# Kernel tuning notes

Hardware: AMD Instinct MI355X
Metric: run time of the kernel (lower is better)

## Reference

```python
import jax, jax.numpy as jnp
import numpy as np

B, T, H, IN, OUT, FUT = 256, 512, 512, 1, 1, 16


def setup_inputs() -> dict:
    key = jax.random.key(0)
    ks = jax.random.split(key, 11)
    bound = 1.0 / np.sqrt(H)  # torch LSTMCell/Linear default init
    u = lambda kk, sh: jax.random.uniform(kk, sh, jnp.float32, -bound, bound)
    fbias = lambda b: b.at[H:2 * H].set(1.0)  # forget-gate bias filled with 1.0 per __init__
    return {
        "x": jax.random.normal(ks[0], (B, T), jnp.float32),
        "Wih0": u(ks[1], (4 * H, IN)),
        "Whh0": u(ks[2], (4 * H, H)),
        "bih0": fbias(u(ks[3], (4 * H,))),
        "bhh0": fbias(u(ks[4], (4 * H,))),
        "Wih1": u(ks[5], (4 * H, H)),
        "Whh1": u(ks[6], (4 * H, H)),
        "bih1": fbias(u(ks[7], (4 * H,))),
        "bhh1": fbias(u(ks[8], (4 * H,))),
        "Wlin": u(ks[9], (OUT, H)),
        "blin": u(ks[10], (OUT,)),
        "future": FUT,
    }


def _cell(xv, h, c, Wih, Whh, bih, bhh):
    # torch.nn.LSTMCell: gates ordered (i, f, g, o)
    gates = xv @ Wih.T + h @ Whh.T + bih + bhh
    i, f, g, o = jnp.split(gates, 4, axis=-1)
    c = jax.nn.sigmoid(f) * c + jax.nn.sigmoid(i) * jnp.tanh(g)
    h = jax.nn.sigmoid(o) * jnp.tanh(c)
    return h, c


def reference(x, Wih0, Whh0, bih0, bhh0, Wih1, Whh1, bih1, bhh1, Wlin, blin, future):
    params = ((Wih0, Whh0, bih0, bhh0), (Wih1, Whh1, bih1, bhh1))
    Bsz, hid = x.shape[0], Whh0.shape[1]
    h0 = tuple(jnp.zeros((Bsz, hid), x.dtype) for _ in params)
    c0 = tuple(jnp.zeros((Bsz, hid), x.dtype) for _ in params)

    def layer_stack(inp, hs, cs):
        new_h, new_c = [], []
        for j, (Wih, Whh, bih, bhh) in enumerate(params):
            h, c = _cell(inp, hs[j], cs[j], Wih, Whh, bih, bhh)
            new_h.append(h)
            new_c.append(c)
            inp = h
        return tuple(new_h), tuple(new_c), inp

    def cond_step(carry, xt):  # xt: [B, 1]
        hs, cs = carry
        hs, cs, top = layer_stack(xt, hs, cs)
        out = top @ Wlin.T + blin  # [B, 1]
        return (hs, cs), out

    xs = jnp.swapaxes(x, 0, 1)[:, :, None]  # [T, B, 1]
    (hs, cs), outs = jax.lax.scan(cond_step, (h0, c0), xs)
    last = outs[-1]

    def fut_step(carry, _):
        hs, cs, out = carry
        hs, cs, top = layer_stack(out, hs, cs)
        out = top @ Wlin.T + blin
        return (hs, cs, out), out

    _, fut_outs = jax.lax.scan(fut_step, (hs, cs, last), None, length=future)

    all_outs = jnp.concatenate([outs, fut_outs], axis=0)  # [T+future, B, 1]
    return jnp.swapaxes(all_outs, 0, 1)[:, :, 0]  # [B, T+future]
```

## Files before the change

kernel.cpp:

```cpp
#include <hip/hip_runtime.h>
#include <hip/hip_bf16.h>
#include <math.h>

#define HID    512
#define BATCH  256
#define TLEN   512
#define FUT    16
#define NSTEP  (TLEN + FUT)
#define NGRP   16
#define WPG    16
#define BPG    16
#define UPW    32
#define NR     128

#define OFF_W0   0u
#define OFF_W1   2097152u
#define OFF_CA   6291456u
#define OFF_XF   7340032u
#define OFF_WI   7357440u
#define OFF_B0   7365632u
#define OFF_B1   7373824u
#define OFF_BAR  7382016u
#define OFF_XT   7384064u

typedef __bf16 bf16x8 __attribute__((ext_vector_type(8)));
typedef float  f32x4  __attribute__((ext_vector_type(4)));

__device__ __forceinline__ float sigf(float v)      { return 1.f / (1.f + __expf(-v)); }
__device__ __forceinline__ float tanh_fast(float v) { return 2.f / (1.f + __expf(-2.f * v)) - 1.f; }

__device__ __forceinline__ void store_short_llc(void* p, unsigned short v) {
    asm volatile("global_store_short %0, %1, off sc0 sc1"
                 :: "v"(p), "v"((unsigned)v) : "memory");
}
__device__ __forceinline__ void gl2lds16_llc(const void* g, void* l) {
    __builtin_amdgcn_global_load_lds(
        (const __attribute__((address_space(1))) void*)g,
        (__attribute__((address_space(3))) void*)l, 16, 0, 17);
}
__device__ __forceinline__ void store_short_l2(void* p, unsigned short v) {
    asm volatile("global_store_short %0, %1, off sc0"
                 :: "v"(p), "v"((unsigned)v) : "memory");
}
__device__ __forceinline__ void gl2lds16_l2(const void* g, void* l) {
    __builtin_amdgcn_global_load_lds(
        (const __attribute__((address_space(1))) void*)g,
        (__attribute__((address_space(3))) void*)l, 16, 0, 1);
}
__device__ __forceinline__ void store_u32_l2(unsigned* p, unsigned v) {
    asm volatile("global_store_dword %0, %1, off sc0" :: "v"(p), "v"(v) : "memory");
}
__device__ __forceinline__ unsigned load_u32_l2(const unsigned* p) {
    unsigned v;
    asm volatile("global_load_dword %0, %1, off sc0\n\t"
                 "s_waitcnt vmcnt(0)" : "=v"(v) : "v"(p) : "memory");
    return v;
}

__device__ __forceinline__ void flag_barrier(unsigned* flags, int m, unsigned phase) {
    __builtin_amdgcn_s_waitcnt(0);
    __syncthreads();
    if (threadIdx.x == 0)
        __hip_atomic_store(&flags[m], phase, __ATOMIC_RELAXED, __HIP_MEMORY_SCOPE_AGENT);
    if (threadIdx.x < 64) {
        const int lane = threadIdx.x;
        const bool active = (lane < WPG) && (lane != m);
        int it = 0;
        for (;;) {
            unsigned f = phase;
            if (active)
                f = __hip_atomic_load(&flags[lane], __ATOMIC_RELAXED, __HIP_MEMORY_SCOPE_AGENT);
            if (__ballot(f >= phase) == ~0ull) break;
            if (++it > 4) __builtin_amdgcn_s_sleep(1);
        }
    }
    __syncthreads();
}

__global__ void lstm_init(char* __restrict__ ws, float* __restrict__ out,
                          const float* __restrict__ blin)
{
    float bl = blin[0];
    int tid = blockIdx.x * blockDim.x + threadIdx.x;
    int stride = gridDim.x * blockDim.x;
    uint4* ca = (uint4*)(ws + OFF_CA);
    for (int i = tid; i < 65536; i += stride) ca[i] = make_uint4(0u, 0u, 0u, 0u);
    float* xf = (float*)(ws + OFF_XF);
    for (int i = tid; i < (FUT + 1) * BATCH; i += stride) xf[i] = bl;
    unsigned* bar = (unsigned*)(ws + OFF_BAR);
    for (int i = tid; i < NGRP * 32; i += stride) bar[i] = 0u;
    for (int i = tid; i < BATCH * NSTEP; i += stride) out[i] = bl;
}

__device__ __forceinline__ int packed_row(int r, int m) {
    return (r & 3) * HID + m * UPW + ((r >> 4) << 2) + ((r >> 2) & 3);
}

__global__ void lstm_pack(char* __restrict__ ws,
    const float* __restrict__ x,
    const float* __restrict__ Wih0, const float* __restrict__ Whh0,
    const float* __restrict__ bih0, const float* __restrict__ bhh0,
    const float* __restrict__ Wih1, const float* __restrict__ Whh1,
    const float* __restrict__ bih1, const float* __restrict__ bhh1)
{
    int tid = blockIdx.x * blockDim.x + threadIdx.x;
    int stride = gridDim.x * blockDim.x;

    __hip_bfloat16* W0p = (__hip_bfloat16*)(ws + OFF_W0);
    for (int i = tid; i < 16 * 128 * 512; i += stride) {
        int k = i & 511, r = (i >> 9) & 127, m = i >> 16;
        int row = packed_row(r, m);
        W0p[i] = __float2bfloat16(Whh0[(size_t)row * HID + k]);
    }
    __hip_bfloat16* W1p = (__hip_bfloat16*)(ws + OFF_W1);
    for (int i = tid; i < 16 * 128 * 1024; i += stride) {
        int k = i & 1023, r = (i >> 10) & 127, m = i >> 17;
        int row = packed_row(r, m);
        float v = (k < 512) ? Wih1[(size_t)row * HID + k] : Whh1[(size_t)row * HID + (k - 512)];
        W1p[i] = __float2bfloat16(v);
    }
    float* wi = (float*)(ws + OFF_WI);
    float* b0 = (float*)(ws + OFF_B0);
    float* b1 = (float*)(ws + OFF_B1);
    for (int i = tid; i < 16 * 128; i += stride) {
        int r = i & 127, m = i >> 7;
        int row = packed_row(r, m);
        wi[i] = Wih0[row];
        b0[i] = bih0[row] + bhh0[row];
        b1[i] = bih1[row] + bhh1[row];
    }
    float* xT = (float*)(ws + OFF_XT);
    for (int i = tid; i < TLEN * BATCH; i += stride) {
        int t = i >> 8, b = i & 255;
        xT[i] = x[(size_t)b * TLEN + t];
    }
}

__global__ __attribute__((amdgpu_flat_work_group_size(512, 512),
                          amdgpu_waves_per_eu(2, 2)))
void lstm_persist(
    const float* __restrict__ wlin,
    float* __restrict__ out, char* __restrict__ ws)
{
    const int tid  = threadIdx.x;
    const int lane = tid & 63;
    const int wave = tid >> 6;
    const int g    = blockIdx.x & 15;
    const int m    = blockIdx.x >> 4;
    const int bbase = g * BPG;

    __shared__ __attribute__((aligned(16))) __hip_bfloat16 As[16 * 1024];
    __shared__ float poS[8][17];
    __shared__ int l2okS;
    char* AsB = (char*)As;

    {
        int* az = (int*)As;
        for (int i = tid; i < (16 * 1024 * 2) / 4; i += 512) az[i] = 0;
    }

    const float* wis = (const float*)(ws + OFF_WI) + m * NR;
    const float* b0s = (const float*)(ws + OFF_B0) + m * NR;
    const float* b1s = (const float*)(ws + OFF_B1) + m * NR;
    char* CAg = ws + OFF_CA + (size_t)g * 65536;
    float* xfeed = (float*)(ws + OFF_XF);
    const float* xT = (const float*)(ws + OFF_XT);
    unsigned* flags = (unsigned*)(ws + OFF_BAR) + g * 32;
    unsigned* tok   = flags + 16;

    const int fl = lane & 15;
    const int fq = lane >> 4;
    const int uloc = wave * 4 + fq;

    const float4 wiV = *(const float4*)(wis + wave * 16 + fq * 4);
    const float4 b0V = *(const float4*)(b0s + wave * 16 + fq * 4);
    const float4 b1V = *(const float4*)(b1s + wave * 16 + fq * 4);
    const float wl0  = wlin[m * UPW + uloc];
    float c00 = 0.f, c10 = 0.f;

    const int cgr  = 4 * m + (uloc >> 3);
    const int pub0 = fl * 1024 + (((cgr + fl) & 63) << 4) + (uloc & 7) * 2;

    const bf16x8* W0row = (const bf16x8*)(ws + OFF_W0 + (size_t)m * NR * 512 * 2)
                          + (size_t)(wave * 16 + fl) * 64;
    const bf16x8* W1row = (const bf16x8*)(ws + OFF_W1 + (size_t)m * NR * 1024 * 2)
                          + (size_t)(wave * 16 + fl) * 128;
    bf16x8 w0f[16], w1f[32];
#pragma unroll
    for (int ks = 0; ks < 16; ++ks) w0f[ks] = W0row[ks * 4 + fq];
#pragma unroll
    for (int ks = 0; ks < 32; ++ks) w1f[ks] = W1row[ks * 4 + fq];

    __syncthreads();

    unsigned phase = 0;
    {
        if (tid == 0) store_u32_l2(&tok[m], 0xA5000000u | (unsigned)m);
        ++phase; flag_barrier(flags, m, phase);
        if (tid < 64) {
            const bool act = (tid < WPG);
            unsigned v = act ? load_u32_l2(&tok[tid]) : 0u;
            int eq = act ? (v == (0xA5000000u | (unsigned)tid)) : 1;
            unsigned long long bal = __ballot(eq);
            if (tid == 0) l2okS = (bal == ~0ull) ? 1 : 0;
        }
        __syncthreads();
        if (tid == 0) store_u32_l2(&tok[m], 0x5A110000u | (unsigned)m);
        ++phase; flag_barrier(flags, m, phase);
        if (tid < 64) {
            const bool act = (tid < WPG);
            unsigned v = act ? load_u32_l2(&tok[tid]) : 0u;
            int eq = act ? (v == (0x5A110000u | (unsigned)tid)) : 1;
            unsigned long long bal = __ballot(eq);
            if (tid == 0 && bal != ~0ull) l2okS = 0;
        }
        __syncthreads();
    }
    const bool l2ok = (l2okS != 0);

    const bf16x8* Asv = (const bf16x8*)As;

    for (int t = 0; t < NSTEP; ++t) {
        const int p = t & 1;
        char* CAp = CAg + p * 32768;
        char* CAq = CAg + (1 - p) * 32768;

        float xv0;
        if (t < TLEN) {
            xv0 = xT[t * BATCH + bbase + fl];
        } else {
            xv0 = xfeed[(t - TLEN) * BATCH + bbase + fl];
        }

        f32x4 aA = {0.f, 0.f, 0.f, 0.f};
        f32x4 aB = {0.f, 0.f, 0.f, 0.f};
#pragma unroll
        for (int j = 0; j < 8; ++j) {
            bf16x8 a0 = Asv[fl * 128 + ((j * 4 + fq + fl) & 63)];
            aA = __builtin_amdgcn_mfma_f32_16x16x32_bf16(w0f[j], a0, aA, 0, 0, 0);
        }
#pragma unroll
        for (int j = 8; j < 16; ++j) {
            bf16x8 a0 = Asv[fl * 128 + ((j * 4 + fq + fl) & 63)];
            aB = __builtin_amdgcn_mfma_f32_16x16x32_bf16(w0f[j], a0, aB, 0, 0, 0);
        }

        {
            float gi = aA[0] + aB[0] + b0V.x + xv0 * wiV.x;
            float gf = aA[1] + aB[1] + b0V.y + xv0 * wiV.y;
            float gg = aA[2] + aB[2] + b0V.z + xv0 * wiV.z;
            float go = aA[3] + aB[3] + b0V.w + xv0 * wiV.w;
            c00 = sigf(gf) * c00 + sigf(gi) * tanh_fast(gg);
            __hip_bfloat16 h = __float2bfloat16(sigf(go) * tanh_fast(c00));
            if (l2ok) store_short_l2 (CAp + pub0, *(unsigned short*)&h);
            else      store_short_llc(CAp + pub0, *(unsigned short*)&h);
        }

        ++phase;
        flag_barrier(flags, m, phase);

        {
#pragma unroll
            for (int ci = 0; ci < 2; ++ci) {
                int b = wave * 2 + ci;
                if (l2ok) {
                    gl2lds16_l2 (CAp + b * 1024 + lane * 16,
                                 AsB + b * 2048 + lane * 16);
                    gl2lds16_l2 (CAq + 16384 + b * 1024 + lane * 16,
                                 AsB + b * 2048 + 1024 + lane * 16);
                } else {
                    gl2lds16_llc(CAp + b * 1024 + lane * 16,
                                 AsB + b * 2048 + lane * 16);
                    gl2lds16_llc(CAq + 16384 + b * 1024 + lane * 16,
                                 AsB + b * 2048 + 1024 + lane * 16);
                }
            }
            __builtin_amdgcn_s_waitcnt(0);
            __syncthreads();
        }

        aA = (f32x4){0.f, 0.f, 0.f, 0.f};
        aB = (f32x4){0.f, 0.f, 0.f, 0.f};
#pragma unroll
        for (int j = 0; j < 16; ++j) {
            bf16x8 a0 = Asv[fl * 128 + ((j * 4 + fq + fl) & 63)];
            aA = __builtin_amdgcn_mfma_f32_16x16x32_bf16(w1f[j], a0, aA, 0, 0, 0);
        }
#pragma unroll
        for (int j = 16; j < 32; ++j) {
            bf16x8 a0 = Asv[fl * 128 + 64 + (((j - 16) * 4 + fq + fl) & 63)];
            aB = __builtin_amdgcn_mfma_f32_16x16x32_bf16(w1f[j], a0, aB, 0, 0, 0);
        }

        {
            float gi = aA[0] + aB[0] + b1V.x;
            float gf = aA[1] + aB[1] + b1V.y;
            float gg = aA[2] + aB[2] + b1V.z;
            float go = aA[3] + aB[3] + b1V.w;
            c10 = sigf(gf) * c10 + sigf(gi) * tanh_fast(gg);
            float h = sigf(go) * tanh_fast(c10);
            __hip_bfloat16 hb = __float2bfloat16(h);
            if (l2ok) store_short_l2 (CAp + 16384 + pub0, *(unsigned short*)&hb);
            else      store_short_llc(CAp + 16384 + pub0, *(unsigned short*)&hb);
            float po = wl0 * h;
            po += __shfl_xor(po, 16, 64);
            po += __shfl_xor(po, 32, 64);
            if (lane < 16) poS[wave][lane] = po;
        }
        __syncthreads();

        if (wave == 0 && lane < 16) {
            float s = poS[0][lane] + poS[1][lane] + poS[2][lane] + poS[3][lane]
                    + poS[4][lane] + poS[5][lane] + poS[6][lane] + poS[7][lane];
            atomicAdd(&out[(size_t)(bbase + lane) * NSTEP + t], s);
            if (t >= TLEN - 1)
                atomicAdd(&xfeed[(t - (TLEN - 1)) * BATCH + bbase + lane], s);
        }

        if (t >= TLEN - 1) {
            ++phase;
            flag_barrier(flags, m, phase);
        }
    }
}

extern "C" void kernel_launch(void* const* d_in, const int* in_sizes, int n_in,
                              void* d_out, int out_size, void* d_ws, size_t ws_size,
                              hipStream_t stream)
{
    const float* x    = (const float*)d_in[0];
    const float* Wih0 = (const float*)d_in[1];
    const float* Whh0 = (const float*)d_in[2];
    const float* bih0 = (const float*)d_in[3];
    const float* bhh0 = (const float*)d_in[4];
    const float* Wih1 = (const float*)d_in[5];
    const float* Whh1 = (const float*)d_in[6];
    const float* bih1 = (const float*)d_in[7];
    const float* bhh1 = (const float*)d_in[8];
    const float* Wlin = (const float*)d_in[9];
    const float* blin = (const float*)d_in[10];
    float* out = (float*)d_out;
    char* ws = (char*)d_ws;

    hipLaunchKernelGGL(lstm_init, dim3(256), dim3(256), 0, stream, ws, out, blin);
    hipLaunchKernelGGL(lstm_pack, dim3(512), dim3(256), 0, stream,
                       ws, x, Wih0, Whh0, bih0, bhh0, Wih1, Whh1, bih1, bhh1);
    hipLaunchKernelGGL(lstm_persist, dim3(256), dim3(512), 0, stream, Wlin, out, ws);
}
```

Before: 1.995 ms.

## Split LSTM gate matvec across waves by K-halves and defer output reduction

Each wave now computes two 16-unit gate tiles over half of the K dimension instead of one tile over all of K. Partial sums from the upper K-half waves go through LDS to the lower half, which applies the nonlinearities. This gives two independent MFMA accumulation chains per wave, so the dependent MFMA chain per step is half as long, at the cost of an extra LDS exchange and __syncthreads per layer, and half the waves sit idle during the activation phase. For the non-feedback steps, the output projection reduction and atomicAdd are moved into the next step's load window so they overlap the global-to-LDS copy, with poS double-buffered to make this safe.

Result: slower. 2.911 ms (+46.0%).

```diff
diff --git a/kernel.cpp b/kernel.cpp
--- a/kernel.cpp
+++ b/kernel.cpp
@@ -150,7 +150,9 @@
     const int bbase = g * BPG;
 
     __shared__ __attribute__((aligned(16))) __hip_bfloat16 As[16 * 1024];
-    __shared__ float poS[8][17];
+    __shared__ __attribute__((aligned(16))) float ppA[8][256];
+    __shared__ __attribute__((aligned(16))) float ppB[8][256];
+    __shared__ float poS[2][4][17];
     __shared__ int l2okS;
     char* AsB = (char*)As;
 
@@ -170,26 +172,38 @@
 
     const int fl = lane & 15;
     const int fq = lane >> 4;
-    const int uloc = wave * 4 + fq;
-
-    const float4 wiV = *(const float4*)(wis + wave * 16 + fq * 4);
-    const float4 b0V = *(const float4*)(b0s + wave * 16 + fq * 4);
-    const float4 b1V = *(const float4*)(b1s + wave * 16 + fq * 4);
-    const float wl0  = wlin[m * UPW + uloc];
-    float c00 = 0.f, c10 = 0.f;
-
-    const int cgr  = 4 * m + (uloc >> 3);
-    const int pub0 = fl * 1024 + (((cgr + fl) & 63) << 4) + (uloc & 7) * 2;
-
-    const bf16x8* W0row = (const bf16x8*)(ws + OFF_W0 + (size_t)m * NR * 512 * 2)
-                          + (size_t)(wave * 16 + fl) * 64;
-    const bf16x8* W1row = (const bf16x8*)(ws + OFF_W1 + (size_t)m * NR * 1024 * 2)
-                          + (size_t)(wave * 16 + fl) * 128;
-    bf16x8 w0f[16], w1f[32];
-#pragma unroll
-    for (int ks = 0; ks < 16; ++ks) w0f[ks] = W0row[ks * 4 + fq];
-#pragma unroll
-    for (int ks = 0; ks < 32; ++ks) w1f[ks] = W1row[ks * 4 + fq];
+    const int kh = wave >> 2;
+    const int wp = wave & 3;
+
+    float4 wiV[2], b0V[2], b1V[2];
+    float  wl0[2];
+    int    pub[2];
+#pragma unroll
+    for (int t2 = 0; t2 < 2; ++t2) {
+        const int T = 2 * wp + t2;
+        wiV[t2] = *(const float4*)(wis + T * 16 + fq * 4);
+        b0V[t2] = *(const float4*)(b0s + T * 16 + fq * 4);
+        b1V[t2] = *(const float4*)(b1s + T * 16 + fq * 4);
+        const int uloc = T * 4 + fq;
+        wl0[t2] = wlin[m * UPW + uloc];
+        const int cgr = 4 * m + (uloc >> 3);
+        pub[t2] = fl * 1024 + (((cgr + fl) & 63) << 4) + (uloc & 7) * 2;
+    }
+    float c00[2] = {0.f, 0.f}, c10[2] = {0.f, 0.f};
+
+    const bf16x8* W0base = (const bf16x8*)(ws + OFF_W0 + (size_t)m * NR * 512 * 2);
+    const bf16x8* W1base = (const bf16x8*)(ws + OFF_W1 + (size_t)m * NR * 1024 * 2);
+    bf16x8 w0f[2][8], w1f[2][16];
+#pragma unroll
+    for (int t2 = 0; t2 < 2; ++t2) {
+        const int row = (2 * wp + t2) * 16 + fl;
+#pragma unroll
+        for (int j = 0; j < 8; ++j)
+            w0f[t2][j] = W0base[(size_t)row * 64 + (kh * 8 + j) * 4 + fq];
+#pragma unroll
+        for (int j = 0; j < 16; ++j)
+            w1f[t2][j] = W1base[(size_t)row * 128 + (kh * 16 + j) * 4 + fq];
+    }
 
     __syncthreads();
 
@@ -232,92 +246,114 @@
             xv0 = xfeed[(t - TLEN) * BATCH + bbase + fl];
         }
 
-        f32x4 aA = {0.f, 0.f, 0.f, 0.f};
-        f32x4 aB = {0.f, 0.f, 0.f, 0.f};
+        f32x4 acc0 = {0.f, 0.f, 0.f, 0.f};
+        f32x4 acc1 = {0.f, 0.f, 0.f, 0.f};
 #pragma unroll
         for (int j = 0; j < 8; ++j) {
-            bf16x8 a0 = Asv[fl * 128 + ((j * 4 + fq + fl) & 63)];
-            aA = __builtin_amdgcn_mfma_f32_16x16x32_bf16(w0f[j], a0, aA, 0, 0, 0);
-        }
-#pragma unroll
-        for (int j = 8; j < 16; ++j) {
-            bf16x8 a0 = Asv[fl * 128 + ((j * 4 + fq + fl) & 63)];
-            aB = __builtin_amdgcn_mfma_f32_16x16x32_bf16(w0f[j], a0, aB, 0, 0, 0);
-        }
-
-        {
-            float gi = aA[0] + aB[0] + b0V.x + xv0 * wiV.x;
-            float gf = aA[1] + aB[1] + b0V.y + xv0 * wiV.y;
-            float gg = aA[2] + aB[2] + b0V.z + xv0 * wiV.z;
-            float go = aA[3] + aB[3] + b0V.w + xv0 * wiV.w;
-            c00 = sigf(gf) * c00 + sigf(gi) * tanh_fast(gg);
-            __hip_bfloat16 h = __float2bfloat16(sigf(go) * tanh_fast(c00));
-            if (l2ok) store_short_l2 (CAp + pub0, *(unsigned short*)&h);
-            else      store_short_llc(CAp + pub0, *(unsigned short*)&h);
+            bf16x8 a0 = Asv[fl * 128 + ((kh * 32 + j * 4 + fq + fl) & 63)];
+            acc0 = __builtin_amdgcn_mfma_f32_16x16x32_bf16(w0f[0][j], a0, acc0, 0, 0, 0);
+            acc1 = __builtin_amdgcn_mfma_f32_16x16x32_bf16(w0f[1][j], a0, acc1, 0, 0, 0);
+        }
+        if (kh == 1) {
+            *(f32x4*)&ppA[wp * 2 + 0][lane * 4] = acc0;
+            *(f32x4*)&ppA[wp * 2 + 1][lane * 4] = acc1;
+        }
+        __syncthreads();
+
+        if (kh == 0) {
+            f32x4 q0 = *(const f32x4*)&ppA[wp * 2 + 0][lane * 4];
+            f32x4 q1 = *(const f32x4*)&ppA[wp * 2 + 1][lane * 4];
+            acc0 += q0; acc1 += q1;
+#pragma unroll
+            for (int t2 = 0; t2 < 2; ++t2) {
+                f32x4 a = t2 ? acc1 : acc0;
+                float gi = a[0] + b0V[t2].x + xv0 * wiV[t2].x;
+                float gf = a[1] + b0V[t2].y + xv0 * wiV[t2].y;
+                float gg = a[2] + b0V[t2].z + xv0 * wiV[t2].z;
+                float go = a[3] + b0V[t2].w + xv0 * wiV[t2].w;
+                c00[t2] = sigf(gf) * c00[t2] + sigf(gi) * tanh_fast(gg);
+                __hip_bfloat16 h = __float2bfloat16(sigf(go) * tanh_fast(c00[t2]));
+                if (l2ok) store_short_l2 (CAp + pub[t2], *(unsigned short*)&h);
+                else      store_short_llc(CAp + pub[t2], *(unsigned short*)&h);
+            }
         }
 
         ++phase;
         flag_barrier(flags, m, phase);
 
-        {
-#pragma unroll
-            for (int ci = 0; ci < 2; ++ci) {
-                int b = wave * 2 + ci;
-                if (l2ok) {
-                    gl2lds16_l2 (CAp + b * 1024 + lane * 16,
-                                 AsB + b * 2048 + lane * 16);
-                    gl2lds16_l2 (CAq + 16384 + b * 1024 + lane * 16,
-                                 AsB + b * 2048 + 1024 + lane * 16);
-                } else {
-                    gl2lds16_llc(CAp + b * 1024 + lane * 16,
-                                 AsB + b * 2048 + lane * 16);
-                    gl2lds16_llc(CAq + 16384 + b * 1024 + lane * 16,
-                                 AsB + b * 2048 + 1024 + lane * 16);
-                }
-            }
-            __builtin_amdgcn_s_waitcnt(0);
-            __syncthreads();
-        }
-
-        aA = (f32x4){0.f, 0.f, 0.f, 0.f};
-        aB = (f32x4){0.f, 0.f, 0.f, 0.f};
+#pragma unroll
+        for (int ci = 0; ci < 2; ++ci) {
+            int b = wave * 2 + ci;
+            if (l2ok) {
+                gl2lds16_l2 (CAp + b * 1024 + lane * 16,
+                             AsB + b * 2048 + lane * 16);
+                gl2lds16_l2 (CAq + 16384 + b * 1024 + lane * 16,
+                             AsB + b * 2048 + 1024 + lane * 16);
+            } else {
+                gl2lds16_llc(CAp + b * 1024 + lane * 16,
+                             AsB + b * 2048 + lane * 16);
+                gl2lds16_llc(CAq + 16384 + b * 1024 + lane * 16,
+                             AsB + b * 2048 + 1024 + lane * 16);
+            }
+        }
+        if (t >= 1 && t < TLEN) {
+            if (wave == 0 && lane < 16) {
+                const int q = (t - 1) & 1;
+                float s = poS[q][0][lane] + poS[q][1][lane]
+                        + poS[q][2][lane] + poS[q][3][lane];
+                atomicAdd(&out[(size_t)(bbase + lane) * NSTEP + (t - 1)], s);
+            }
+        }
+        __builtin_amdgcn_s_waitcnt(0);
+        __syncthreads();
+
+        acc0 = (f32x4){0.f, 0.f, 0.f, 0.f};
+        acc1 = (f32x4){0.f, 0.f, 0.f, 0.f};
 #pragma unroll
         for (int j = 0; j < 16; ++j) {
-            bf16x8 a0 = Asv[fl * 128 + ((j * 4 + fq + fl) & 63)];
-            aA = __builtin_amdgcn_mfma_f32_16x16x32_bf16(w1f[j], a0, aA, 0, 0, 0);
-        }
-#pragma unroll
-        for (int j = 16; j < 32; ++j) {
-            bf16x8 a0 = Asv[fl * 128 + 64 + (((j - 16) * 4 + fq + fl) & 63)];
-            aB = __builtin_amdgcn_mfma_f32_16x16x32_bf16(w1f[j], a0, aB, 0, 0, 0);
-        }
-
-        {
-            float gi = aA[0] + aB[0] + b1V.x;
-            float gf = aA[1] + aB[1] + b1V.y;
-            float gg = aA[2] + aB[2] + b1V.z;
-            float go = aA[3] + aB[3] + b1V.w;
-            c10 = sigf(gf) * c10 + sigf(gi) * tanh_fast(gg);
-            float h = sigf(go) * tanh_fast(c10);
-            __hip_bfloat16 hb = __float2bfloat16(h);
-            if (l2ok) store_short_l2 (CAp + 16384 + pub0, *(unsigned short*)&hb);
-            else      store_short_llc(CAp + 16384 + pub0, *(unsigned short*)&hb);
-            float po = wl0 * h;
+            bf16x8 a0 = Asv[fl * 128 + kh * 64 + ((j * 4 + fq + fl) & 63)];
+            acc0 = __builtin_amdgcn_mfma_f32_16x16x32_bf16(w1f[0][j], a0, acc0, 0, 0, 0);
+            acc1 = __builtin_amdgcn_mfma_f32_16x16x32_bf16(w1f[1][j], a0, acc1, 0, 0, 0);
+        }
+        if (kh == 1) {
+            *(f32x4*)&ppB[wp * 2 + 0][lane * 4] = acc0;
+            *(f32x4*)&ppB[wp * 2 + 1][lane * 4] = acc1;
+        }
+        __syncthreads();
+
+        if (kh == 0) {
+            f32x4 q0 = *(const f32x4*)&ppB[wp * 2 + 0][lane * 4];
+            f32x4 q1 = *(const f32x4*)&ppB[wp * 2 + 1][lane * 4];
+            acc0 += q0; acc1 += q1;
+            float po = 0.f;
+#pragma unroll
+            for (int t2 = 0; t2 < 2; ++t2) {
+                f32x4 a = t2 ? acc1 : acc0;
+                float gi = a[0] + b1V[t2].x;
+                float gf = a[1] + b1V[t2].y;
+                float gg = a[2] + b1V[t2].z;
+                float go = a[3] + b1V[t2].w;
+                c10[t2] = sigf(gf) * c10[t2] + sigf(gi) * tanh_fast(gg);
+                float h = sigf(go) * tanh_fast(c10[t2]);
+                __hip_bfloat16 hb = __float2bfloat16(h);
+                if (l2ok) store_short_l2 (CAp + 16384 + pub[t2], *(unsigned short*)&hb);
+                else      store_short_llc(CAp + 16384 + pub[t2], *(unsigned short*)&hb);
+                po += wl0[t2] * h;
+            }
             po += __shfl_xor(po, 16, 64);
             po += __shfl_xor(po, 32, 64);
-            if (lane < 16) poS[wave][lane] = po;
-        }
-        __syncthreads();
-
-        if (wave == 0 && lane < 16) {
-            float s = poS[0][lane] + poS[1][lane] + poS[2][lane] + poS[3][lane]
-                    + poS[4][lane] + poS[5][lane] + poS[6][lane] + poS[7][lane];
-            atomicAdd(&out[(size_t)(bbase + lane) * NSTEP + t], s);
-            if (t >= TLEN - 1)
+            if (lane < 16) poS[t & 1][wp][lane] = po;
+        }
+
+        if (t >= TLEN - 1) {
+            __syncthreads();
+            if (wave == 0 && lane < 16) {
+                const int q = t & 1;
+                float s = poS[q][0][lane] + poS[q][1][lane]
+                        + poS[q][2][lane] + poS[q][3][lane];
+                atomicAdd(&out[(size_t)(bbase + lane) * NSTEP + t], s);
                 atomicAdd(&xfeed[(t - (TLEN - 1)) * BATCH + bbase + lane], s);
-        }
-
-        if (t >= TLEN - 1) {
+            }
             ++phase;
             flag_barrier(flags, m, phase);
         }
```
